# Optimization experiments

Measured on AMD Instinct MI355X. Metric: run time of the kernel, lower is better.

Reference implementation:

```python
import jax, jax.numpy as jnp
import numpy as np

L, H = 2, 512  # num_layers, hidden_dim (== input_dim)

def setup_inputs() -> dict:
    key = jax.random.key(0)
    ks = jax.random.split(key, 9)
    T, B, D = 1024, 64, 512
    s = 0.05  # scale randn params to keep gates non-saturated
    return {
        "x":   jax.random.normal(ks[0], (T, B, D), jnp.float32),
        "Wii": jax.random.normal(ks[1], (L, 3 * H, D), jnp.float32) * s,
        "Wic": jax.random.normal(ks[2], (L, 3 * H, H), jnp.float32) * s,
        "Wih": jax.random.normal(ks[3], (L, 3 * H, H), jnp.float32) * s,
        "bii": jax.random.normal(ks[4], (L, 3 * H), jnp.float32) * s,
        "bic": jax.random.normal(ks[5], (L, 3 * H), jnp.float32) * s,
        "bih": jax.random.normal(ks[6], (L, 3 * H), jnp.float32) * s,
        "Whh": jax.random.normal(ks[7], (L, H, H), jnp.float32) * s,
        "bhh": jax.random.normal(ks[8], (L, H), jnp.float32) * s,
    }

def _res_lstm_layer(xs, Wii, Wic, Wih, bii, bic, bih, Whh, bhh):
    # xs: [T, B, D]; input_size == hidden_size so residual is identity add.
    T, B, _ = xs.shape
    bias = bii + bic + bih  # fold the three gate biases once
    def step(carry, x_t):
        hx, cx = carry
        gates = (jnp.matmul(x_t, Wii.T) + jnp.matmul(hx, Wih.T)
                 + jnp.matmul(cx, Wic.T) + bias)          # [B, 3H]
        i_g, f_g, o_g = jnp.split(gates, 3, axis=1)
        cellgate = jnp.tanh(jnp.matmul(hx, Whh.T) + bhh)    # [B, H]
        cy = jax.nn.sigmoid(f_g) * cx + jax.nn.sigmoid(i_g) * cellgate
        hy = jax.nn.sigmoid(o_g) * (jnp.tanh(cy) + x_t)     # residual
        return (hy, cy), hy
    init = (jnp.zeros((B, H), xs.dtype), jnp.zeros((B, H), xs.dtype))
    (h, c), outs = jax.lax.scan(step, init, xs)
    return outs, h, c

def reference(x, Wii, Wic, Wih, bii, bic, bih, Whh, bhh):
    outs = x
    h_list, c_list = [], []
    for l in range(L):  # small fixed layer count
        outs, h, c = _res_lstm_layer(outs, Wii[l], Wic[l], Wih[l],
                                     bii[l], bic[l], bih[l], Whh[l], bhh[l])
        h_list.append(h)
        c_list.append(c)
    h_n = jnp.stack(h_list, axis=0)  # [L, B, H]
    c_n = jnp.stack(c_list, axis=0)
    return outs, h_n, c_n
```

## Files before the change

### kernel.cpp

```cpp
#include <hip/hip_runtime.h>
#include <cstdint>

typedef unsigned short u16;
typedef unsigned int   u32;
typedef __bf16 v8bf  __attribute__((ext_vector_type(8)));
typedef float  v4f   __attribute__((ext_vector_type(4)));
typedef u32    u32x2 __attribute__((ext_vector_type(2)));
typedef u32    u32x4 __attribute__((ext_vector_type(4)));

#define T_STEPS 1024
#define G3 1536

#define OFF_RING0 0ull
#define OFF_RING1 1048576ull
#define OFF_XBF   0ull
#define OFF_XG    67108864ull
#define OFF_WII   268435456ull
#define OFF_WPACK 270008320ull
#define OFF_WPK2  277348352ull
#define OFF_BIASF 278921216ull

__device__ __forceinline__ u16 f2b(float f) {
  u32 u = __builtin_bit_cast(u32, f);
  u += 0x7fffu + ((u >> 16) & 1u);
  return (u16)(u >> 16);
}
__device__ __forceinline__ float b2f(u16 h) {
  u32 u = ((u32)h) << 16;
  return __builtin_bit_cast(float, u);
}
__device__ __forceinline__ float sigm(float x) { return 1.0f / (1.0f + __expf(-x)); }


__global__ void k_cvt(const float* __restrict__ s, u16* __restrict__ d, int n4) {
  int i = blockIdx.x * blockDim.x + threadIdx.x;
  int st = gridDim.x * blockDim.x;
  for (; i < n4; i += st) {
    float4 v = reinterpret_cast<const float4*>(s)[i];
    u32 lo = (u32)f2b(v.x) | ((u32)f2b(v.y) << 16);
    u32 hi = (u32)f2b(v.z) | ((u32)f2b(v.w) << 16);
    uint2 pk; pk.x = lo; pk.y = hi;
    reinterpret_cast<uint2*>(d)[i] = pk;
  }
}

__global__ void k_fold(const float* __restrict__ a, const float* __restrict__ b,
                       const float* __restrict__ c, float* __restrict__ o, int n) {
  int i = blockIdx.x * blockDim.x + threadIdx.x;
  if (i < n) o[i] = a[i] + b[i] + c[i];
}

__global__ void k_pack(const float* __restrict__ Wih, const float* __restrict__ Wic,
                       const float* __restrict__ Whh, u16* __restrict__ wp) {
  int t = blockIdx.x * blockDim.x + threadIdx.x;
  if (t >= 2 * 32 * 112 * 64) return;
  int lane = t & 63; int rest = t >> 6;
  int c = rest % 112; rest /= 112;
  int s = rest & 31; int l = rest >> 5;
  int col16 = lane & 15, kq = lane >> 4;
  const float* src;
  if (c < 96) {
    int tau = c >> 5, kk = c & 31;
    int col = tau * 512 + s * 16 + col16;
    int k = kk * 32 + kq * 8;
    src = (k < 512) ? (Wih + ((size_t)l * G3 + col) * 512 + k)
                    : (Wic + ((size_t)l * G3 + col) * 512 + (k - 512));
  } else {
    int kk = c - 96;
    int col = s * 16 + col16;
    int k = kk * 32 + kq * 8;
    src = Whh + ((size_t)l * 512 + col) * 512 + k;
  }
  u16 o[8];
#pragma unroll
  for (int i = 0; i < 8; ++i) o[i] = f2b(src[i]);
  uint4 v;
  v.x = (u32)o[0] | ((u32)o[1] << 16);
  v.y = (u32)o[2] | ((u32)o[3] << 16);
  v.z = (u32)o[4] | ((u32)o[5] << 16);
  v.w = (u32)o[6] | ((u32)o[7] << 16);
  reinterpret_cast<uint4*>(wp)[t] = v;
}

__global__ void k_pack2(const float* __restrict__ Wii, u16* __restrict__ wp2) {
  int t = blockIdx.x * blockDim.x + threadIdx.x;
  if (t >= 32 * 3 * 16 * 64) return;
  int lane = t & 63;
  int kk = (t >> 6) & 15;
  int w = (t >> 10) % 3;
  int s = t / 3072;
  int col = w * 512 + s * 16 + (lane & 15);
  int k = kk * 32 + (lane >> 4) * 8;
  const float* src = Wii + ((size_t)G3 + col) * 512 + k;
  u16 o[8];
#pragma unroll
  for (int i = 0; i < 8; ++i) o[i] = f2b(src[i]);
  uint4 v;
  v.x = (u32)o[0] | ((u32)o[1] << 16);
  v.y = (u32)o[2] | ((u32)o[3] << 16);
  v.z = (u32)o[4] | ((u32)o[5] << 16);
  v.w = (u32)o[6] | ((u32)o[7] << 16);
  reinterpret_cast<uint4*>(wp2)[t] = v;
}


__global__ __launch_bounds__(256) void k_gemm(const u16* __restrict__ A,
                                              const u16* __restrict__ Bt,
                                              u16* __restrict__ C) {
  __shared__ u16 As[128 * 40];
  __shared__ u16 Bs[128 * 40];
  int m0 = blockIdx.x * 128, n0 = blockIdx.y * 128;
  int tid = threadIdx.x, lane = tid & 63, w = tid >> 6, wr = w >> 1, wc = w & 1;
  int rl = lane & 15, kq = lane >> 4;
  v4f acc[4][4] = {};
  for (int k0 = 0; k0 < 512; k0 += 32) {
#pragma unroll
    for (int c = tid; c < 1024; c += 256) {
      int row = (c & 511) >> 2, q = c & 3;
      const u16* src = (c < 512) ? (A + (size_t)(m0 + row) * 512 + k0 + q * 8)
                                 : (Bt + (size_t)(n0 + row) * 512 + k0 + q * 8);
      uint4 v = *reinterpret_cast<const uint4*>(src);
      u16* dst = (c < 512) ? (As + row * 40 + q * 8) : (Bs + row * 40 + q * 8);
      *reinterpret_cast<uint4*>(dst) = v;
    }
    __syncthreads();
    v8bf a[4], b[4];
#pragma unroll
    for (int mi = 0; mi < 4; ++mi)
      a[mi] = *reinterpret_cast<const v8bf*>(As + (wr * 64 + mi * 16 + rl) * 40 + kq * 8);
#pragma unroll
    for (int ni = 0; ni < 4; ++ni)
      b[ni] = *reinterpret_cast<const v8bf*>(Bs + (wc * 64 + ni * 16 + rl) * 40 + kq * 8);
#pragma unroll
    for (int mi = 0; mi < 4; ++mi)
#pragma unroll
      for (int ni = 0; ni < 4; ++ni)
        acc[mi][ni] = __builtin_amdgcn_mfma_f32_16x16x32_bf16(a[mi], b[ni], acc[mi][ni], 0, 0, 0);
    __syncthreads();
  }
#pragma unroll
  for (int mi = 0; mi < 4; ++mi)
#pragma unroll
    for (int ni = 0; ni < 4; ++ni)
#pragma unroll
      for (int r = 0; r < 4; ++r) {
        int row = m0 + wr * 64 + mi * 16 + kq * 4 + r;
        int col = n0 + wc * 64 + ni * 16 + rl;
        C[(size_t)row * G3 + col] = f2b(acc[mi][ni][r]);
      }
}


__global__ __launch_bounds__(512, 1) void k_lstm(
    const u16* __restrict__ xg, const u16* __restrict__ wp, const u16* __restrict__ wp2,
    const float* __restrict__ biasf, const float* __restrict__ bhh,
    const float* __restrict__ xin, float* __restrict__ outs,
    float* __restrict__ hn, float* __restrict__ cn,
    char* __restrict__ ring0, char* __restrict__ ring1) {
  extern __shared__ char lds[];
  u16* alds   = (u16*)lds;
  float* olds = (float*)(lds + 65792);
  u16* w1lds  = (u16*)(lds + 73984);
  int tid = threadIdx.x, lane = tid & 63, w = tid >> 6;
  int w2 = w >> 1, half = w & 1;
  int blk = blockIdx.x, g = blk >> 5, s = blk & 31;

  int erow = (tid >> 4) & 15, ecol = tid & 15;
  int bglob = g * 16 + erow, hcol = s * 16 + ecol;
  int col16 = lane & 15, kq = lane >> 4;
  bool isGate = (w2 < 3);
  float bias0 = 0.0f, bias1 = 0.0f;
  int cbase, nch;
  if (isGate) {
    cbase = w2 * 32 + half * 16; nch = 16;
    if (half == 0) {
      bias0 = biasf[w2 * 512 + s * 16 + col16];
      bias1 = biasf[1536 + w2 * 512 + s * 16 + col16];
    }
  } else {
    cbase = 96 + half * 8; nch = 8;
    if (half == 0) {
      bias0 = bhh[s * 16 + col16];
      bias1 = bhh[512 + s * 16 + col16];
    }
  }
  int colglob = w2 * 512 + s * 16 + col16;

  const u16* w0src = wp + (size_t)s * 57344 + (size_t)cbase * 512 + lane * 8;
  const u16* w1src = wp + 1835008 + (size_t)s * 57344 + (size_t)cbase * 512 + lane * 8;
  v8bf breg0[16], breg1[16];
  if (isGate) {
#pragma unroll
    for (int kk = 0; kk < 16; ++kk) {
      breg0[kk] = *reinterpret_cast<const v8bf*>(w0src + kk * 512);
      breg1[kk] = *reinterpret_cast<const v8bf*>(w1src + kk * 512);
    }
  } else {
#pragma unroll
    for (int kk = 0; kk < 8; ++kk) {
      breg0[kk] = *reinterpret_cast<const v8bf*>(w0src + kk * 512);
      breg1[kk] = *reinterpret_cast<const v8bf*>(w1src + kk * 512);
    }
  }
  {
    const uint4* src = reinterpret_cast<const uint4*>(wp2) + (size_t)s * 3072;
    for (int i = tid; i < 3072; i += 512)
      reinterpret_cast<uint4*>(w1lds)[i] = src[i];
  }
  float c0 = 0.0f, c1 = 0.0f;
  __syncthreads();

  auto Af = [&](int base, int kg) {
    return *reinterpret_cast<const v8bf*>(alds + col16 * 2056 + base + kg * 32 + kq * 8);
  };

  for (int t = 0; t <= T_STEPS; ++t) {
    bool doL0 = (t < T_STEPS), doL1 = (t > 0);

    float seed0[4] = {0.f, 0.f, 0.f, 0.f};
    float xi0 = 0.0f;
    if (doL0) {
      if (isGate) {
        if (half == 0) {
          const u16* xgp = xg + (size_t)(t * 64 + g * 16 + kq * 4) * G3 + colglob;
#pragma unroll
          for (int r4 = 0; r4 < 4; ++r4) seed0[r4] = b2f(xgp[(size_t)r4 * G3]) + bias0;
        }
      } else if (half == 0) {
#pragma unroll
        for (int r4 = 0; r4 < 4; ++r4) seed0[r4] = bias0;
      }
      if (tid < 256) xi0 = xin[(size_t)(t * 64 + bglob) * 512 + hcol];
    }

    u32x4 r[8];
    {
      const char* pb = ring0 + ((size_t)(t & 3) * 4 + g) * 65536 + (size_t)tid * 16;
      u32 exp = (u32)t; bool ok = false; u32 it = 0;
      while (!ok) {
#pragma unroll
        for (int i = 0; i < 8; ++i)
          asm volatile("global_load_dwordx4 %0, %1, off sc0 sc1"
                       : "=v"(r[i]) : "v"(pb + (size_t)i * 8192) : "memory");
        asm volatile("s_waitcnt vmcnt(0)" ::: "memory");
        __builtin_amdgcn_sched_barrier(0);
        ok = true;
#pragma unroll
        for (int i = 0; i < 8; ++i) ok = ok && (r[i][1] == exp) && (r[i][3] == exp);
        if (!ok) { if (++it > (1u << 11)) break; __builtin_amdgcn_s_sleep(1); }
      }
      __builtin_amdgcn_sched_barrier(0);
#pragma unroll
      for (int i = 0; i < 8; ++i) {
        int p = tid + i * 512;
        int row = p >> 8, c2 = p & 255;
        u32 hw = (r[i][0] & 0xffffu) | (r[i][2] << 16);
        u32 cw = (r[i][0] >> 16) | (r[i][2] & 0xffff0000u);
        *reinterpret_cast<u32*>(alds + row * 2056 + 2 * c2) = hw;
        *reinterpret_cast<u32*>(alds + row * 2056 + 512 + 2 * c2) = cw;
      }
    }

    u32x4 r2[8];
    if (doL1) {
      const char* pb = ring1 + ((size_t)((t - 1) & 3) * 4 + g) * 65536 + (size_t)tid * 16;
#pragma unroll
      for (int i = 0; i < 8; ++i)
        asm volatile("global_load_dwordx4 %0, %1, off sc0 sc1"
                     : "=v"(r2[i]) : "v"(pb + (size_t)i * 8192) : "memory");
    }
    __syncthreads();

    if (doL0) {
      v4f ac0, ac1, ac2, ac3;
#pragma unroll
      for (int r4 = 0; r4 < 4; ++r4) { ac0[r4] = seed0[r4]; ac1[r4] = 0.f; ac2[r4] = 0.f; ac3[r4] = 0.f; }
      if (isGate) {
#pragma unroll
        for (int kk = 0; kk < 16; kk += 4) {
          int kg = half * 16 + kk;
          ac0 = __builtin_amdgcn_mfma_f32_16x16x32_bf16(Af(0, kg + 0), breg0[kk + 0], ac0, 0, 0, 0);
          ac1 = __builtin_amdgcn_mfma_f32_16x16x32_bf16(Af(0, kg + 1), breg0[kk + 1], ac1, 0, 0, 0);
          ac2 = __builtin_amdgcn_mfma_f32_16x16x32_bf16(Af(0, kg + 2), breg0[kk + 2], ac2, 0, 0, 0);
          ac3 = __builtin_amdgcn_mfma_f32_16x16x32_bf16(Af(0, kg + 3), breg0[kk + 3], ac3, 0, 0, 0);
        }
      } else {
#pragma unroll
        for (int kk = 0; kk < 8; kk += 4) {
          int kg = half * 8 + kk;
          ac0 = __builtin_amdgcn_mfma_f32_16x16x32_bf16(Af(0, kg + 0), breg0[kk + 0], ac0, 0, 0, 0);
          ac1 = __builtin_amdgcn_mfma_f32_16x16x32_bf16(Af(0, kg + 1), breg0[kk + 1], ac1, 0, 0, 0);
          ac2 = __builtin_amdgcn_mfma_f32_16x16x32_bf16(Af(0, kg + 2), breg0[kk + 2], ac2, 0, 0, 0);
          ac3 = __builtin_amdgcn_mfma_f32_16x16x32_bf16(Af(0, kg + 3), breg0[kk + 3], ac3, 0, 0, 0);
        }
      }
      v4f acc;
#pragma unroll
      for (int r4 = 0; r4 < 4; ++r4) acc[r4] = (ac0[r4] + ac1[r4]) + (ac2[r4] + ac3[r4]);
#pragma unroll
      for (int r4 = 0; r4 < 4; ++r4) olds[w * 256 + (kq * 4 + r4) * 16 + col16] = acc[r4];
      __syncthreads();

      if (tid < 256) {
        float gi = olds[tid] + olds[256 + tid];
        float gf = olds[512 + tid] + olds[768 + tid];
        float go = olds[1024 + tid] + olds[1280 + tid];
        float gg = olds[1536 + tid] + olds[1792 + tid];
        float i_s = sigm(gi), f_s = sigm(gf), o_s = sigm(go);
        float cg = tanhf(gg);
        float cy = f_s * c0 + i_s * cg;
        float hy = o_s * (tanhf(cy) + xi0);
        c0 = cy;
        u16 hyb = f2b(hy), cyb = f2b(cy);
        u32x2 pkt;
        pkt[0] = (u32)hyb | ((u32)cyb << 16);
        pkt[1] = (u32)(t + 1);
        void* pd = ring0 + ((size_t)((t + 1) & 3) * 4 + g) * 65536
                   + (size_t)(erow * 512 + hcol) * 8;
        asm volatile("global_store_dwordx2 %0, %1, off sc0 sc1"
                     :: "v"(pd), "v"(pkt) : "memory");
        if (t == T_STEPS - 1) {
          hn[bglob * 512 + hcol] = hy;
          cn[bglob * 512 + hcol] = cy;
        }
      }
    }

    if (doL1) {
      float xi1 = (tid < 256) ? b2f(alds[erow * 2056 + hcol]) : 0.0f;

      {
        const char* pb = ring1 + ((size_t)((t - 1) & 3) * 4 + g) * 65536 + (size_t)tid * 16;
        u32 exp = (u32)(t - 1); u32 it = 0;
        for (;;) {
          asm volatile("s_waitcnt vmcnt(0)" ::: "memory");
          __builtin_amdgcn_sched_barrier(0);
          bool ok = true;
#pragma unroll
          for (int i = 0; i < 8; ++i) ok = ok && (r2[i][1] == exp) && (r2[i][3] == exp);
          if (ok) break;
          if (++it > (1u << 11)) break;
          __builtin_amdgcn_s_sleep(1);
#pragma unroll
          for (int i = 0; i < 8; ++i)
            asm volatile("global_load_dwordx4 %0, %1, off sc0 sc1"
                         : "=v"(r2[i]) : "v"(pb + (size_t)i * 8192) : "memory");
        }
        __builtin_amdgcn_sched_barrier(0);
#pragma unroll
        for (int i = 0; i < 8; ++i) {
          int p = tid + i * 512;
          int row = p >> 8, c2 = p & 255;
          u32 hw = (r2[i][0] & 0xffffu) | (r2[i][2] << 16);
          u32 cw = (r2[i][0] >> 16) | (r2[i][2] & 0xffff0000u);
          *reinterpret_cast<u32*>(alds + row * 2056 + 1024 + 2 * c2) = hw;
          *reinterpret_cast<u32*>(alds + row * 2056 + 1536 + 2 * c2) = cw;
        }
      }
      __syncthreads();

      v4f ac0, ac1, ac2, ac3;
#pragma unroll
      for (int r4 = 0; r4 < 4; ++r4) { ac0[r4] = bias1; ac1[r4] = 0.f; ac2[r4] = 0.f; ac3[r4] = 0.f; }
      if (isGate) {
#pragma unroll
        for (int kk = 0; kk < 16; kk += 4) {
          int kg = half * 16 + kk;
          ac0 = __builtin_amdgcn_mfma_f32_16x16x32_bf16(Af(1024, kg + 0), breg1[kk + 0], ac0, 0, 0, 0);
          ac1 = __builtin_amdgcn_mfma_f32_16x16x32_bf16(Af(1024, kg + 1), breg1[kk + 1], ac1, 0, 0, 0);
          ac2 = __builtin_amdgcn_mfma_f32_16x16x32_bf16(Af(1024, kg + 2), breg1[kk + 2], ac2, 0, 0, 0);
          ac3 = __builtin_amdgcn_mfma_f32_16x16x32_bf16(Af(1024, kg + 3), breg1[kk + 3], ac3, 0, 0, 0);
        }
#pragma unroll
        for (int kx = 0; kx < 8; kx += 4) {
          int kg = half * 8 + kx;
          ac0 = __builtin_amdgcn_mfma_f32_16x16x32_bf16(Af(0, kg + 0),
                  *reinterpret_cast<const v8bf*>(w1lds + ((w2 * 16 + kg + 0) * 64 + lane) * 8), ac0, 0, 0, 0);
          ac1 = __builtin_amdgcn_mfma_f32_16x16x32_bf16(Af(0, kg + 1),
                  *reinterpret_cast<const v8bf*>(w1lds + ((w2 * 16 + kg + 1) * 64 + lane) * 8), ac1, 0, 0, 0);
          ac2 = __builtin_amdgcn_mfma_f32_16x16x32_bf16(Af(0, kg + 2),
                  *reinterpret_cast<const v8bf*>(w1lds + ((w2 * 16 + kg + 2) * 64 + lane) * 8), ac2, 0, 0, 0);
          ac3 = __builtin_amdgcn_mfma_f32_16x16x32_bf16(Af(0, kg + 3),
                  *reinterpret_cast<const v8bf*>(w1lds + ((w2 * 16 + kg + 3) * 64 + lane) * 8), ac3, 0, 0, 0);
        }
      } else {
#pragma unroll
        for (int kk = 0; kk < 8; kk += 4) {
          int kg = half * 8 + kk;
          ac0 = __builtin_amdgcn_mfma_f32_16x16x32_bf16(Af(1024, kg + 0), breg1[kk + 0], ac0, 0, 0, 0);
          ac1 = __builtin_amdgcn_mfma_f32_16x16x32_bf16(Af(1024, kg + 1), breg1[kk + 1], ac1, 0, 0, 0);
          ac2 = __builtin_amdgcn_mfma_f32_16x16x32_bf16(Af(1024, kg + 2), breg1[kk + 2], ac2, 0, 0, 0);
          ac3 = __builtin_amdgcn_mfma_f32_16x16x32_bf16(Af(1024, kg + 3), breg1[kk + 3], ac3, 0, 0, 0);
        }
      }
      v4f acc;
#pragma unroll
      for (int r4 = 0; r4 < 4; ++r4) acc[r4] = (ac0[r4] + ac1[r4]) + (ac2[r4] + ac3[r4]);
#pragma unroll
      for (int r4 = 0; r4 < 4; ++r4) olds[w * 256 + (kq * 4 + r4) * 16 + col16] = acc[r4];
      __syncthreads();

      if (tid < 256) {
        float gi = olds[tid] + olds[256 + tid];
        float gf = olds[512 + tid] + olds[768 + tid];
        float go = olds[1024 + tid] + olds[1280 + tid];
        float gg = olds[1536 + tid] + olds[1792 + tid];
        float i_s = sigm(gi), f_s = sigm(gf), o_s = sigm(go);
        float cg = tanhf(gg);
        float cy = f_s * c1 + i_s * cg;
        float hy = o_s * (tanhf(cy) + xi1);
        c1 = cy;
        u16 hyb = f2b(hy), cyb = f2b(cy);
        u32x2 pkt;
        pkt[0] = (u32)hyb | ((u32)cyb << 16);
        pkt[1] = (u32)t;
        void* pd = ring1 + ((size_t)(t & 3) * 4 + g) * 65536
                   + (size_t)(erow * 512 + hcol) * 8;
        asm volatile("global_store_dwordx2 %0, %1, off sc0 sc1"
                     :: "v"(pd), "v"(pkt) : "memory");
        outs[(size_t)((t - 1) * 64 + bglob) * 512 + hcol] = hy;
        if (t == T_STEPS) {
          hn[32768 + bglob * 512 + hcol] = hy;
          cn[32768 + bglob * 512 + hcol] = cy;
        }
      }
    }
    __syncthreads();
  }
}


extern "C" void kernel_launch(void* const* d_in, const int* in_sizes, int n_in,
                              void* d_out, int out_size, void* d_ws, size_t ws_size,
                              hipStream_t stream) {
  const float* x   = (const float*)d_in[0];
  const float* Wii = (const float*)d_in[1];
  const float* Wic = (const float*)d_in[2];
  const float* Wih = (const float*)d_in[3];
  const float* bii = (const float*)d_in[4];
  const float* bic = (const float*)d_in[5];
  const float* bih = (const float*)d_in[6];
  const float* Whh = (const float*)d_in[7];
  const float* bhh = (const float*)d_in[8];
  float* out = (float*)d_out;
  char* ws = (char*)d_ws;

  u16* xbf     = (u16*)(ws + OFF_XBF);
  u16* xgb     = (u16*)(ws + OFF_XG);
  u16* wiib    = (u16*)(ws + OFF_WII);
  u16* wpack   = (u16*)(ws + OFF_WPACK);
  u16* wpk2    = (u16*)(ws + OFF_WPK2);
  float* biasf = (float*)(ws + OFF_BIASF);

  hipFuncSetAttribute(reinterpret_cast<const void*>(k_lstm),
                      hipFuncAttributeMaxDynamicSharedMemorySize, 123136);

  k_cvt <<<2048, 256, 0, stream>>>(x, xbf, 8388608);
  k_cvt <<<768, 256, 0, stream>>>(Wii, wiib, 196608);
  k_fold<<<12, 256, 0, stream>>>(bii, bic, bih, biasf, 3072);
  k_pack<<<1792, 256, 0, stream>>>(Wih, Wic, Whh, wpack);
  k_pack2<<<384, 256, 0, stream>>>(Wii, wpk2);
  k_gemm<<<dim3(512, 12), 256, 0, stream>>>(xbf, wiib, xgb);

  hipMemsetAsync(ws + OFF_RING0, 0, 2097152, stream);

  float* hn = out + 33554432;
  float* cn = out + 33554432 + 65536;
  k_lstm<<<128, 512, 123136, stream>>>(
      xgb, wpack, wpk2, biasf, bhh, x, out, hn, cn,
      ws + OFF_RING0, ws + OFF_RING1);
}
```

Baseline: 5.538 ms.

## Prefetch next-step ring and xg/x loads, use lighter LDS-only barriers

Result: faster. 5.315 ms (-4.0%).

```diff
diff --git a/kernel.cpp b/kernel.cpp
--- a/kernel.cpp
+++ b/kernel.cpp
@@ -30,6 +30,10 @@
   return __builtin_bit_cast(float, u);
 }
 __device__ __forceinline__ float sigm(float x) { return 1.0f / (1.0f + __expf(-x)); }
+
+__device__ __forceinline__ void bar_lds() {
+  asm volatile("s_waitcnt lgkmcnt(0)\n\ts_barrier" ::: "memory");
+}
 
 
 __global__ void k_cvt(const float* __restrict__ s, u16* __restrict__ d, int n4) {
@@ -170,21 +174,30 @@
   int col16 = lane & 15, kq = lane >> 4;
   bool isGate = (w2 < 3);
   float bias0 = 0.0f, bias1 = 0.0f;
-  int cbase, nch;
+  int cbase;
   if (isGate) {
-    cbase = w2 * 32 + half * 16; nch = 16;
+    cbase = w2 * 32 + half * 16;
     if (half == 0) {
       bias0 = biasf[w2 * 512 + s * 16 + col16];
       bias1 = biasf[1536 + w2 * 512 + s * 16 + col16];
     }
   } else {
-    cbase = 96 + half * 8; nch = 8;
+    cbase = 96 + half * 8;
     if (half == 0) {
       bias0 = bhh[s * 16 + col16];
       bias1 = bhh[512 + s * 16 + col16];
     }
   }
   int colglob = w2 * 512 + s * 16 + col16;
+
+  u32x4 rA[8];
+  {
+    const char* pb = ring0 + (size_t)g * 65536 + (size_t)tid * 16;
+#pragma unroll
+    for (int i = 0; i < 8; ++i)
+      asm volatile("global_load_dwordx4 %0, %1, off sc0 sc1"
+                   : "=v"(rA[i]) : "v"(pb + (size_t)i * 8192) : "memory");
+  }
 
   const u16* w0src = wp + (size_t)s * 57344 + (size_t)cbase * 512 + lane * 8;
   const u16* w1src = wp + 1835008 + (size_t)s * 57344 + (size_t)cbase * 512 + lane * 8;
@@ -207,6 +220,15 @@
     for (int i = tid; i < 3072; i += 512)
       reinterpret_cast<uint4*>(w1lds)[i] = src[i];
   }
+  float pre_s0 = 0.f, pre_s1 = 0.f, pre_s2 = 0.f, pre_s3 = 0.f, pre_xi = 0.f;
+  if (isGate && half == 0) {
+    const u16* xgp = xg + (size_t)(g * 16 + kq * 4) * G3 + colglob;
+    pre_s0 = b2f(xgp[0]);
+    pre_s1 = b2f(xgp[(size_t)G3]);
+    pre_s2 = b2f(xgp[(size_t)2 * G3]);
+    pre_s3 = b2f(xgp[(size_t)3 * G3]);
+  }
+  if (tid < 256) pre_xi = xin[(size_t)bglob * 512 + hcol];
   float c0 = 0.0f, c1 = 0.0f;
   __syncthreads();
 
@@ -220,42 +242,44 @@
     float seed0[4] = {0.f, 0.f, 0.f, 0.f};
     float xi0 = 0.0f;
     if (doL0) {
-      if (isGate) {
-        if (half == 0) {
-          const u16* xgp = xg + (size_t)(t * 64 + g * 16 + kq * 4) * G3 + colglob;
-#pragma unroll
-          for (int r4 = 0; r4 < 4; ++r4) seed0[r4] = b2f(xgp[(size_t)r4 * G3]) + bias0;
-        }
-      } else if (half == 0) {
-#pragma unroll
-        for (int r4 = 0; r4 < 4; ++r4) seed0[r4] = bias0;
-      }
-      if (tid < 256) xi0 = xin[(size_t)(t * 64 + bglob) * 512 + hcol];
-    }
-
-    u32x4 r[8];
+      if (half == 0) {
+        if (isGate) {
+          seed0[0] = pre_s0 + bias0; seed0[1] = pre_s1 + bias0;
+          seed0[2] = pre_s2 + bias0; seed0[3] = pre_s3 + bias0;
+        } else {
+#pragma unroll
+          for (int r4 = 0; r4 < 4; ++r4) seed0[r4] = bias0;
+        }
+      }
+      if (tid < 256) xi0 = pre_xi;
+    }
+
     {
       const char* pb = ring0 + ((size_t)(t & 3) * 4 + g) * 65536 + (size_t)tid * 16;
-      u32 exp = (u32)t; bool ok = false; u32 it = 0;
-      while (!ok) {
+      u32 exp = (u32)t, it = 0;
+      asm volatile("s_waitcnt vmcnt(0)" ::: "memory");
+      __builtin_amdgcn_sched_barrier(0);
+      for (;;) {
+        bool ok = true;
+#pragma unroll
+        for (int i = 0; i < 8; ++i) ok = ok && (rA[i][1] == exp) && (rA[i][3] == exp);
+        if (ok) break;
+        if (++it > (1u << 11)) break;
+        __builtin_amdgcn_s_sleep(1);
 #pragma unroll
         for (int i = 0; i < 8; ++i)
           asm volatile("global_load_dwordx4 %0, %1, off sc0 sc1"
-                       : "=v"(r[i]) : "v"(pb + (size_t)i * 8192) : "memory");
+                       : "=v"(rA[i]) : "v"(pb + (size_t)i * 8192) : "memory");
         asm volatile("s_waitcnt vmcnt(0)" ::: "memory");
         __builtin_amdgcn_sched_barrier(0);
-        ok = true;
-#pragma unroll
-        for (int i = 0; i < 8; ++i) ok = ok && (r[i][1] == exp) && (r[i][3] == exp);
-        if (!ok) { if (++it > (1u << 11)) break; __builtin_amdgcn_s_sleep(1); }
       }
       __builtin_amdgcn_sched_barrier(0);
 #pragma unroll
       for (int i = 0; i < 8; ++i) {
         int p = tid + i * 512;
         int row = p >> 8, c2 = p & 255;
-        u32 hw = (r[i][0] & 0xffffu) | (r[i][2] << 16);
-        u32 cw = (r[i][0] >> 16) | (r[i][2] & 0xffff0000u);
+        u32 hw = (rA[i][0] & 0xffffu) | (rA[i][2] << 16);
+        u32 cw = (rA[i][0] >> 16) | (rA[i][2] & 0xffff0000u);
         *reinterpret_cast<u32*>(alds + row * 2056 + 2 * c2) = hw;
         *reinterpret_cast<u32*>(alds + row * 2056 + 512 + 2 * c2) = cw;
       }
@@ -269,7 +293,7 @@
         asm volatile("global_load_dwordx4 %0, %1, off sc0 sc1"
                      : "=v"(r2[i]) : "v"(pb + (size_t)i * 8192) : "memory");
     }
-    __syncthreads();
+    bar_lds();
 
     if (doL0) {
       v4f ac0, ac1, ac2, ac3;
@@ -299,7 +323,7 @@
       for (int r4 = 0; r4 < 4; ++r4) acc[r4] = (ac0[r4] + ac1[r4]) + (ac2[r4] + ac3[r4]);
 #pragma unroll
       for (int r4 = 0; r4 < 4; ++r4) olds[w * 256 + (kq * 4 + r4) * 16 + col16] = acc[r4];
-      __syncthreads();
+      bar_lds();
 
       if (tid < 256) {
         float gi = olds[tid] + olds[256 + tid];
@@ -331,10 +355,11 @@
 
       {
         const char* pb = ring1 + ((size_t)((t - 1) & 3) * 4 + g) * 65536 + (size_t)tid * 16;
-        u32 exp = (u32)(t - 1); u32 it = 0;
+        u32 exp = (u32)(t - 1), it = 0;
+        if (doL0 && w < 4) asm volatile("s_waitcnt vmcnt(1)" ::: "memory");
+        else               asm volatile("s_waitcnt vmcnt(0)" ::: "memory");
+        __builtin_amdgcn_sched_barrier(0);
         for (;;) {
-          asm volatile("s_waitcnt vmcnt(0)" ::: "memory");
-          __builtin_amdgcn_sched_barrier(0);
           bool ok = true;
 #pragma unroll
           for (int i = 0; i < 8; ++i) ok = ok && (r2[i][1] == exp) && (r2[i][3] == exp);
@@ -345,6 +370,8 @@
           for (int i = 0; i < 8; ++i)
             asm volatile("global_load_dwordx4 %0, %1, off sc0 sc1"
                          : "=v"(r2[i]) : "v"(pb + (size_t)i * 8192) : "memory");
+          asm volatile("s_waitcnt vmcnt(0)" ::: "memory");
+          __builtin_amdgcn_sched_barrier(0);
         }
         __builtin_amdgcn_sched_barrier(0);
 #pragma unroll
@@ -357,7 +384,7 @@
           *reinterpret_cast<u32*>(alds + row * 2056 + 1536 + 2 * c2) = cw;
         }
       }
-      __syncthreads();
+      bar_lds();
 
       v4f ac0, ac1, ac2, ac3;
 #pragma unroll
@@ -398,7 +425,7 @@
       for (int r4 = 0; r4 < 4; ++r4) acc[r4] = (ac0[r4] + ac1[r4]) + (ac2[r4] + ac3[r4]);
 #pragma unroll
       for (int r4 = 0; r4 < 4; ++r4) olds[w * 256 + (kq * 4 + r4) * 16 + col16] = acc[r4];
-      __syncthreads();
+      bar_lds();
 
       if (tid < 256) {
         float gi = olds[tid] + olds[256 + tid];
@@ -425,7 +452,25 @@
         }
       }
     }
-    __syncthreads();
+
+    if (t + 1 < T_STEPS) {
+      if (isGate && half == 0) {
+        const u16* xgp = xg + (size_t)((t + 1) * 64 + g * 16 + kq * 4) * G3 + colglob;
+        pre_s0 = b2f(xgp[0]);
+        pre_s1 = b2f(xgp[(size_t)G3]);
+        pre_s2 = b2f(xgp[(size_t)2 * G3]);
+        pre_s3 = b2f(xgp[(size_t)3 * G3]);
+      }
+      if (tid < 256) pre_xi = xin[(size_t)((t + 1) * 64 + bglob) * 512 + hcol];
+    }
+    if (t < T_STEPS) {
+      const char* pb0 = ring0 + ((size_t)((t + 1) & 3) * 4 + g) * 65536 + (size_t)tid * 16;
+#pragma unroll
+      for (int i = 0; i < 8; ++i)
+        asm volatile("global_load_dwordx4 %0, %1, off sc0 sc1"
+                     : "=v"(rA[i]) : "v"(pb0 + (size_t)i * 8192) : "memory");
+    }
+    bar_lds();
   }
 }
 
```
